# Optimization experiments

Measured on AMD Instinct MI355X. Metric: run time of the kernel, lower is better.

## Reference

```python
import jax, jax.numpy as jnp
import numpy as np

H, W = 48, 48
L = H * W            # 2304 tokens
D = 256              # d_model
NH = 8               # heads (self and memory attn)
FF = 1024            # dim_feedforward
T = 2                # memory frames
BS = 1
GN_GROUPS = 32       # GNActDWConv2d default groups


def layernorm(x, g, b, eps=1e-5):
    m = jnp.mean(x, -1, keepdims=True)
    v = jnp.mean((x - m) ** 2, -1, keepdims=True)
    return (x - m) * jax.lax.rsqrt(v + eps) * g + b


def linear(x, Wt, b):
    # torch nn.Linear convention: Wt is [out, in]
    return x @ Wt.T + b


def mha_core(Q, K, V, nhead):
    # Q [Lq, bs, C], K/V [Lk, bs, C]; AOT MultiheadAttention core (eval: no dropout)
    Lq, bs, C = Q.shape
    hd = C // nhead
    Qh = (Q / np.float32(np.sqrt(hd))).reshape(Lq, bs, nhead, hd).transpose(1, 2, 0, 3)
    Kh = K.reshape(-1, bs, nhead, hd).transpose(1, 2, 0, 3)
    Vh = V.reshape(-1, bs, nhead, hd).transpose(1, 2, 0, 3)
    attn = jax.nn.softmax(jnp.einsum('bhqd,bhkd->bhqk', Qh, Kh), axis=-1)
    out = jnp.einsum('bhqk,bhkd->bhqd', attn, Vh)
    return out.transpose(2, 0, 1, 3).reshape(Lq, bs, C)


def groupnorm(x, g, b, groups, eps=1e-5):
    bs, c, h, w = x.shape
    xg = x.reshape(bs, groups, c // groups, h, w)
    m = jnp.mean(xg, (2, 3, 4), keepdims=True)
    v = jnp.mean((xg - m) ** 2, (2, 3, 4), keepdims=True)
    xg = (xg - m) * jax.lax.rsqrt(v + eps)
    return xg.reshape(bs, c, h, w) * g[None, :, None, None] + b[None, :, None, None]


def dwconv5(x, k):
    # depthwise 5x5, padding=2; x [bs,c,h,w], k [c,1,5,5]
    return jax.lax.conv_general_dilated(x, k, (1, 1), ((2, 2), (2, 2)),
                                        feature_group_count=x.shape[1])


def setup_inputs() -> dict:
    key = jax.random.key(0)
    ks = jax.random.split(key, 16)
    rn = lambda i, shape, s=1.0: jax.random.normal(ks[i], shape, jnp.float32) * s
    w = 0.02
    inp = {
        'tgt': rn(0, (L, BS, D)),
        'global_K': rn(1, (T, L, BS, D)),
        'global_V': rn(2, (T, L, BS, D)),
        'local_K': rn(3, (L, BS, D)),
        'local_V': rn(4, (L, BS, D)),
        # LayerNorms
        'ln1_g': jnp.ones(D, jnp.float32), 'ln1_b': jnp.zeros(D, jnp.float32),
        'ln2_g': jnp.ones(D, jnp.float32), 'ln2_b': jnp.zeros(D, jnp.float32),
        'ln3_g': jnp.ones(D, jnp.float32), 'ln3_b': jnp.zeros(D, jnp.float32),
        'ln4_g': jnp.ones(D, jnp.float32), 'ln4_b': jnp.zeros(D, jnp.float32),
        # self_attn (use_linear=True) Q/K/V + projection
        'sa_Wq': rn(5, (D, D), w), 'sa_bq': jnp.zeros(D, jnp.float32),
        'sa_Wk': rn(6, (D, D), w), 'sa_bk': jnp.zeros(D, jnp.float32),
        'sa_Wv': rn(7, (D, D), w), 'sa_bv': jnp.zeros(D, jnp.float32),
        'sa_Wo': rn(8, (D, D), w), 'sa_bo': jnp.zeros(D, jnp.float32),
        # block linear_Q
        'Wq': rn(9, (D, D), w), 'bq': jnp.zeros(D, jnp.float32),
        # long/short term attn projections (use_linear=False)
        'lt_Wo': rn(10, (D, D), w), 'lt_bo': jnp.zeros(D, jnp.float32),
        'st_Wo': rn(11, (D, D), w), 'st_bo': jnp.zeros(D, jnp.float32),
        # FFN: linear1 -> GN+GELU+DWConv -> linear2
        'W1': rn(12, (FF, D), w), 'b1': jnp.zeros(FF, jnp.float32),
        'gn_g': jnp.ones(FF, jnp.float32), 'gn_b': jnp.zeros(FF, jnp.float32),
        'dw_k': rn(13, (FF, 1, 5, 5), 0.05),
        'W2': rn(14, (D, FF), w), 'b2': jnp.zeros(D, jnp.float32),
    }
    return inp


def reference(tgt, global_K, global_V, local_K, local_V,
              ln1_g, ln1_b, ln2_g, ln2_b, ln3_g, ln3_b, ln4_g, ln4_b,
              sa_Wq, sa_bq, sa_Wk, sa_bk, sa_Wv, sa_bv, sa_Wo, sa_bo,
              Wq, bq, lt_Wo, lt_bo, st_Wo, st_bo,
              W1, b1, gn_g, gn_b, dw_k, W2, b2):
    # --- stage 1: self-attention ---
    _tgt = layernorm(tgt, ln1_g, ln1_b)
    q = linear(_tgt, sa_Wq, sa_bq)
    k = linear(_tgt, sa_Wk, sa_bk)
    v = linear(_tgt, sa_Wv, sa_bv)
    tgt2 = linear(mha_core(q, k, v, NH), sa_Wo, sa_bo)
    tgt = tgt + tgt2  # droppath is identity at eval

    # --- stage 2: long-term + short-term memory cross-attention ---
    _tgt = layernorm(tgt, ln2_g, ln2_b)
    curr_Q = linear(_tgt, Wq, bq)
    curr_K = curr_Q
    curr_V = _tgt

    flat_K = global_K.reshape(-1, BS, D)  # [T*L, bs, D]
    flat_V = global_V.reshape(-1, BS, D)
    tgt2 = linear(mha_core(curr_Q, flat_K, flat_V, NH), lt_Wo, lt_bo)

    k_st = layernorm(local_K + curr_K, ln4_g, ln4_b)
    v_st = layernorm(local_V + curr_V, ln4_g, ln4_b)
    tgt3 = linear(mha_core(curr_Q, k_st, v_st, NH), st_Wo, st_bo)

    tgt = tgt + tgt2 + tgt3

    # --- stage 3: FFN with GN + GELU + depthwise conv ---
    _tgt = layernorm(tgt, ln3_g, ln3_b)
    x = linear(_tgt, W1, b1)                        # [L, bs, FF]
    x = x.reshape(H, W, BS, FF).transpose(2, 3, 0, 1)  # [bs, FF, H, W]
    x = jax.nn.gelu(groupnorm(x, gn_g, gn_b, GN_GROUPS), approximate=False)
    x = dwconv5(x, dw_k)
    x = x.reshape(BS, FF, L).transpose(2, 0, 1)     # [L, bs, FF]
    tgt2 = linear(x, W2, b2)
    return tgt + tgt2
```

## Files before the change

### kernel.cpp

```cpp
#include <hip/hip_runtime.h>
#include <hip/hip_bf16.h>

#define L   2304
#define D   256
#define NHD 8
#define HD  32
#define FF  1024
#define HH  48
#define WWW 48
#define SPL 4
#define RCH 24
#define RP  (L / RCH)
#define S2LOG 0.25503486f

typedef unsigned short bfraw;
typedef __attribute__((ext_vector_type(8))) short s8v;
typedef __attribute__((ext_vector_type(4))) float f4v;

__device__ __forceinline__ bfraw f2b(float x) {
    __hip_bfloat16 h = __float2bfloat16(x);
    return __builtin_bit_cast(bfraw, h);
}

__global__ __launch_bounds__(256) void diag_kernel(float* __restrict__ out, float c, int n)
{
    int i = blockIdx.x * 256 + threadIdx.x;
    if (i < n) out[i] = c;
}

__global__ __launch_bounds__(256) void ln_kernel(
    const float* __restrict__ inA, const float* __restrict__ inB,
    const float* __restrict__ g, const float* __restrict__ b,
    float* __restrict__ out, bfraw* __restrict__ outb)
{
    int row = blockIdx.x, t = threadIdx.x;
    size_t idx = (size_t)row * D + t;
    float v = inA[idx];
    if (inB) v += inB[idx];
    __shared__ float rs[256], rq[256];
    rs[t] = v; rq[t] = v * v;
    __syncthreads();
    for (int o = 128; o > 0; o >>= 1) {
        if (t < o) { rs[t] += rs[t + o]; rq[t] += rq[t + o]; }
        __syncthreads();
    }
    float mean = rs[0] * (1.f / D);
    float var  = rq[0] * (1.f / D) - mean * mean;
    float rstd = rsqrtf(var + 1e-5f);
    float r = (v - mean) * rstd * g[t] + b[t];
    if (out)  out[idx]  = r;
    if (outb) outb[idx] = f2b(r);
}

__global__ __launch_bounds__(256) void gemm_mfma(
    const bfraw* __restrict__ A, const float* __restrict__ W,
    const float* __restrict__ bias, const float* res, float* out,
    bfraw* __restrict__ outb, float oscale,
    int M, int N, int K)
{
    __shared__ __attribute__((aligned(16))) short Wl[64][32];
    int t = threadIdx.x;
    int w = t >> 6, l = t & 63;
    int lo = l & 15, quad = l >> 4;
    int m0 = blockIdx.x * 32, n0 = blockIdx.y * 64;
    int wr = (w & 1) * 16, wc = (w >> 1) * 32;
    f4v acc[2];
    acc[0] = (f4v){0.f, 0.f, 0.f, 0.f};
    acc[1] = (f4v){0.f, 0.f, 0.f, 0.f};

    int aswz = (quad ^ ((lo >> 2) & 3)) * 8;
    int srow = t >> 3, spart = t & 7;
    const bfraw* ap = A + (size_t)(m0 + wr + lo) * K + quad * 8;

    for (int k0 = 0; k0 < K; k0 += 32) {
        float4 w4[2];
        #pragma unroll
        for (int i = 0; i < 2; i++)
            w4[i] = *reinterpret_cast<const float4*>(W + (size_t)(n0 + i * 32 + srow) * K + k0 + spart * 4);
        s8v af = *reinterpret_cast<const s8v*>(ap + k0);
        __syncthreads();
        #pragma unroll
        for (int i = 0; i < 2; i++) {
            int row = i * 32 + srow;
            int col = ((spart >> 1) ^ ((row >> 2) & 3)) * 8 + (spart & 1) * 4;
            ushort4 wb;
            wb.x = f2b(w4[i].x); wb.y = f2b(w4[i].y); wb.z = f2b(w4[i].z); wb.w = f2b(w4[i].w);
            *reinterpret_cast<ushort4*>(&Wl[row][col]) = wb;
        }
        __syncthreads();
        #pragma unroll
        for (int j = 0; j < 2; j++) {
            int rw = wc + j * 16 + lo;
            s8v wf = *reinterpret_cast<const s8v*>(&Wl[rw][aswz]);
            acc[j] = __builtin_amdgcn_mfma_f32_16x16x32_bf16(af, wf, acc[j], 0, 0, 0);
        }
    }

    #pragma unroll
    for (int j = 0; j < 2; j++) {
        #pragma unroll
        for (int r = 0; r < 4; r++) {
            int mrow = m0 + wr + quad * 4 + r;
            int ncol = n0 + wc + j * 16 + lo;
            float v = acc[j][r] + bias[ncol];
            size_t idx = (size_t)mrow * N + ncol;
            if (res) v += res[idx];
            if (out) out[idx] = v;
            if (outb) outb[idx] = f2b(v * oscale);
        }
    }
}

__global__ __launch_bounds__(256) void cvt_kernel(
    const float* __restrict__ in, bfraw* __restrict__ out)
{
    size_t i = ((size_t)blockIdx.x * 256 + threadIdx.x) * 4;
    float4 v = *reinterpret_cast<const float4*>(in + i);
    ushort4 o;
    o.x = f2b(v.x); o.y = f2b(v.y); o.z = f2b(v.z); o.w = f2b(v.w);
    *reinterpret_cast<ushort4*>(out + i) = o;
}

__global__ __launch_bounds__(256) void cvtT_kernel(
    const float* __restrict__ in, bfraw* __restrict__ out, int N)
{
    __shared__ float Ls[32][33];
    int h = blockIdx.y, n0 = blockIdx.x * 32, t = threadIdx.x;
    int nl = t >> 3, dq = t & 7;
    float4 v = *reinterpret_cast<const float4*>(in + (size_t)(n0 + nl) * D + h * HD + dq * 4);
    Ls[nl][dq*4+0] = v.x; Ls[nl][dq*4+1] = v.y;
    Ls[nl][dq*4+2] = v.z; Ls[nl][dq*4+3] = v.w;
    __syncthreads();
    int dl = t >> 3, nq = t & 7;
    ushort4 o;
    o.x = f2b(Ls[nq*4+0][dl]); o.y = f2b(Ls[nq*4+1][dl]);
    o.z = f2b(Ls[nq*4+2][dl]); o.w = f2b(Ls[nq*4+3][dl]);
    *reinterpret_cast<ushort4*>(out + (size_t)(h * HD + dl) * N + n0 + nq * 4) = o;
}

__global__ __launch_bounds__(256) void attn_mfma_split(
    const bfraw* __restrict__ Qb, const bfraw* __restrict__ Kb,
    const bfraw* __restrict__ Vt, float* __restrict__ OP,
    float* __restrict__ ML, int Lk, int chunk)
{
    __shared__ __attribute__((aligned(16))) short Ks[64][32];
    __shared__ __attribute__((aligned(16))) short Vts[32][72];
    __shared__ __attribute__((aligned(16))) short Ps[4][16][72];
    __shared__ float Tb[4][16][33];
    int t = threadIdx.x;
    int w = t >> 6, l = t & 63;
    int h = blockIdx.y, q0 = blockIdx.x * 64 + w * 16, z = blockIdx.z;
    int lo = l & 15, quad = l >> 4;
    int kb = z * chunk, ke = kb + chunk;

    s8v qf = *reinterpret_cast<const s8v*>(Qb + (size_t)(q0 + lo) * D + h * HD + quad * 8);
    int kswz = (quad ^ ((lo >> 2) & 3)) * 8;

    int skey = t >> 2, spart = t & 3;
    int kcol = (spart ^ ((skey >> 2) & 3)) * 8;
    int sd = t >> 3, svp = t & 7;
    const bfraw* kp = Kb + (size_t)skey * D + h * HD + spart * 8;
    const bfraw* vp = Vt + (size_t)(h * HD + sd) * Lk + svp * 8;

    float m_r = -1e30f, l_r = 0.f;
    f4v o0 = {0.f, 0.f, 0.f, 0.f}, o1 = {0.f, 0.f, 0.f, 0.f};

    for (int k0 = kb; k0 < ke; k0 += 64) {
        s8v kv = *reinterpret_cast<const s8v*>(kp + (size_t)k0 * D);
        s8v vv = *reinterpret_cast<const s8v*>(vp + k0);
        __syncthreads();
        *reinterpret_cast<s8v*>(&Ks[skey][kcol]) = kv;
        *reinterpret_cast<s8v*>(&Vts[sd][svp * 8]) = vv;
        __syncthreads();

        f4v sc4[4];
        #pragma unroll
        for (int s = 0; s < 4; s++) {
            s8v kf = *reinterpret_cast<const s8v*>(&Ks[lo + 16 * s][kswz]);
            sc4[s] = __builtin_amdgcn_mfma_f32_16x16x32_bf16(kf, qf, (f4v){0.f,0.f,0.f,0.f}, 0, 0, 0);
        }
        float cm = -1e30f;
        #pragma unroll
        for (int s = 0; s < 4; s++)
            #pragma unroll
            for (int r = 0; r < 4; r++)
                cm = fmaxf(cm, sc4[s][r]);
        cm = fmaxf(cm, __shfl_xor(cm, 16));
        cm = fmaxf(cm, __shfl_xor(cm, 32));
        bool skip = __all(cm <= m_r + 8.f);
        if (!skip) {
            float mnew = fmaxf(m_r, cm);
            float alpha = __builtin_amdgcn_exp2f(m_r - mnew);
            l_r *= alpha;
            #pragma unroll
            for (int r = 0; r < 4; r++) { o0[r] *= alpha; o1[r] *= alpha; }
            m_r = mnew;
        }
        float ls = 0.f;
        #pragma unroll
        for (int s = 0; s < 4; s++) {
            float p0 = __builtin_amdgcn_exp2f(sc4[s][0] - m_r);
            float p1 = __builtin_amdgcn_exp2f(sc4[s][1] - m_r);
            float p2 = __builtin_amdgcn_exp2f(sc4[s][2] - m_r);
            float p3 = __builtin_amdgcn_exp2f(sc4[s][3] - m_r);
            ls += p0 + p1 + p2 + p3;
            ushort4 pk;
            pk.x = f2b(p0); pk.y = f2b(p1); pk.z = f2b(p2); pk.w = f2b(p3);
            *reinterpret_cast<ushort4*>(&Ps[w][lo][s * 16 + quad * 4]) = pk;
        }
        ls += __shfl_xor(ls, 16);
        ls += __shfl_xor(ls, 32);
        l_r += ls;
        #pragma unroll
        for (int kc = 0; kc < 2; kc++) {
            s8v pf = *reinterpret_cast<const s8v*>(&Ps[w][lo][kc * 32 + quad * 8]);
            s8v v0 = *reinterpret_cast<const s8v*>(&Vts[lo][kc * 32 + quad * 8]);
            s8v v1 = *reinterpret_cast<const s8v*>(&Vts[16 + lo][kc * 32 + quad * 8]);
            o0 = __builtin_amdgcn_mfma_f32_16x16x32_bf16(v0, pf, o0, 0, 0, 0);
            o1 = __builtin_amdgcn_mfma_f32_16x16x32_bf16(v1, pf, o1, 0, 0, 0);
        }
    }

    #pragma unroll
    for (int r = 0; r < 4; r++) {
        Tb[w][lo][quad * 4 + r]      = o0[r];
        Tb[w][lo][16 + quad * 4 + r] = o1[r];
    }
    float* Oz = OP + (size_t)z * L * D;
    int ql = l >> 2, dq = (l & 3) * 8;
    float4 u0, u1;
    u0.x = Tb[w][ql][dq + 0]; u0.y = Tb[w][ql][dq + 1];
    u0.z = Tb[w][ql][dq + 2]; u0.w = Tb[w][ql][dq + 3];
    u1.x = Tb[w][ql][dq + 4]; u1.y = Tb[w][ql][dq + 5];
    u1.z = Tb[w][ql][dq + 6]; u1.w = Tb[w][ql][dq + 7];
    *reinterpret_cast<float4*>(Oz + (size_t)(q0 + ql) * D + h * HD + dq)     = u0;
    *reinterpret_cast<float4*>(Oz + (size_t)(q0 + ql) * D + h * HD + dq + 4) = u1;
    if (l < 16) {
        size_t mi = (((size_t)z * NHD + h) * L + q0 + lo) * 2;
        ML[mi]     = m_r;
        ML[mi + 1] = l_r;
    }
}

__global__ __launch_bounds__(256) void attn_combine(
    const float* __restrict__ OP, const float* __restrict__ ML,
    bfraw* __restrict__ Ob)
{
    int q = blockIdx.x, t = threadIdx.x, h = t >> 5;
    float m[SPL], lv[SPL];
    float M = -1e30f;
    #pragma unroll
    for (int s = 0; s < SPL; s++) {
        size_t mi = (((size_t)s * NHD + h) * L + q) * 2;
        m[s]  = ML[mi];
        lv[s] = ML[mi + 1];
        M = fmaxf(M, m[s]);
    }
    float wl = 0.f, acc = 0.f;
    #pragma unroll
    for (int s = 0; s < SPL; s++) {
        float w = __builtin_amdgcn_exp2f(m[s] - M);
        wl  += w * lv[s];
        acc += w * OP[(size_t)s * L * D + (size_t)q * D + t];
    }
    Ob[(size_t)q * D + t] = f2b(acc / wl);
}

__global__ __launch_bounds__(256) void gn_stats_part(
    const float* __restrict__ X, float* __restrict__ ps)
{
    int g = blockIdx.x, rc = blockIdx.y, t = threadIdx.x;
    int cq = (t & 7) * 4;
    int rl = t >> 3;
    int r0 = rc * RP;
    float s = 0.f, sq = 0.f;
    #pragma unroll
    for (int p = 0; p < RP / 32; p++) {
        int l = r0 + p * 32 + rl;
        float4 v = *reinterpret_cast<const float4*>(X + (size_t)l * FF + g * 32 + cq);
        s  += v.x + v.y + v.z + v.w;
        sq += v.x*v.x + v.y*v.y + v.z*v.z + v.w*v.w;
    }
    __shared__ float rs[256], rq[256];
    rs[t] = s; rq[t] = sq;
    __syncthreads();
    for (int o = 128; o > 0; o >>= 1) {
        if (t < o) { rs[t] += rs[t + o]; rq[t] += rq[t + o]; }
        __syncthreads();
    }
    if (t == 0) {
        ps[(g * RCH + rc) * 2]     = rs[0];
        ps[(g * RCH + rc) * 2 + 1] = rq[0];
    }
}

__global__ __launch_bounds__(64) void gn_stats_final(
    const float* __restrict__ ps, float* __restrict__ st)
{
    int g = threadIdx.x;
    if (g < 32) {
        float s = 0.f, sq = 0.f;
        for (int i = 0; i < RCH; i++) {
            s  += ps[(g * RCH + i) * 2];
            sq += ps[(g * RCH + i) * 2 + 1];
        }
        float n = (float)(L * 32);
        float mean = s / n;
        float var  = sq / n - mean * mean;
        st[g * 2]     = mean;
        st[g * 2 + 1] = rsqrtf(var + 1e-5f);
    }
}

__global__ __launch_bounds__(256) void gn_gelu_dwconv(
    const float* __restrict__ X, const float* __restrict__ st,
    const float* __restrict__ gg, const float* __restrict__ gb,
    const float* __restrict__ Kw, bfraw* __restrict__ Y)
{
    __shared__ float tile[144][64];
    int h0 = blockIdx.x * 8, w0 = blockIdx.y * 8, c0 = blockIdx.z * 64;
    int t = threadIdx.x;
    int c = t & 63;
    int cg = (c0 + c) >> 5;
    float mu = st[2 * cg], rs = st[2 * cg + 1];
    float ga = gg[c0 + c], be = gb[c0 + c];

    for (int i = t; i < 144 * 64; i += 256) {
        int sp = i >> 6;
        int hy = h0 + (sp / 12) - 2, wx = w0 + (sp % 12) - 2;
        float v = 0.f;
        if (hy >= 0 && hy < HH && wx >= 0 && wx < WWW) {
            float x = X[(size_t)(hy * WWW + wx) * FF + c0 + c];
            x = (x - mu) * rs * ga + be;
            v = 0.5f * x * (1.f + erff(x * 0.70710678118654752f));
        }
        tile[sp][c] = v;
    }
    float kw[25];
    #pragma unroll
    for (int i = 0; i < 25; i++) kw[i] = Kw[(size_t)(c0 + c) * 25 + i];
    __syncthreads();

    int sgrp = t >> 6;
    for (int s = 0; s < 16; s++) {
        int sp = sgrp * 16 + s;
        int oh = sp >> 3, ow = sp & 7;
        float acc = 0.f;
        #pragma unroll
        for (int ky = 0; ky < 5; ky++)
            #pragma unroll
            for (int kx = 0; kx < 5; kx++)
                acc += tile[(oh + ky) * 12 + ow + kx][c] * kw[ky * 5 + kx];
        Y[(size_t)((h0 + oh) * WWW + w0 + ow) * FF + c0 + c] = f2b(acc);
    }
}

extern "C" void kernel_launch(void* const* d_in, const int* in_sizes, int n_in,
                              void* d_out, int out_size, void* d_ws, size_t ws_size,
                              hipStream_t stream)
{
    (void)in_sizes;
    float* out = (float*)d_out;

    if (n_in != 34) {
        diag_kernel<<<(out_size + 255) / 256, 256, 0, stream>>>(out, 2000.f, out_size);
        return;
    }

    const float* tgt    = (const float*)d_in[0];
    const float* gK     = (const float*)d_in[1];
    const float* gV     = (const float*)d_in[2];
    const float* lK     = (const float*)d_in[3];
    const float* lV     = (const float*)d_in[4];
    const float* ln1_g  = (const float*)d_in[5];
    const float* ln1_b  = (const float*)d_in[6];
    const float* ln2_g  = (const float*)d_in[7];
    const float* ln2_b  = (const float*)d_in[8];
    const float* ln3_g  = (const float*)d_in[9];
    const float* ln3_b  = (const float*)d_in[10];
    const float* ln4_g  = (const float*)d_in[11];
    const float* ln4_b  = (const float*)d_in[12];
    const float* sa_Wq  = (const float*)d_in[13];
    const float* sa_bq  = (const float*)d_in[14];
    const float* sa_Wk  = (const float*)d_in[15];
    const float* sa_bk  = (const float*)d_in[16];
    const float* sa_Wv  = (const float*)d_in[17];
    const float* sa_bv  = (const float*)d_in[18];
    const float* sa_Wo  = (const float*)d_in[19];
    const float* sa_bo  = (const float*)d_in[20];
    const float* Wq     = (const float*)d_in[21];
    const float* bq     = (const float*)d_in[22];
    const float* lt_Wo  = (const float*)d_in[23];
    const float* lt_bo  = (const float*)d_in[24];
    const float* st_Wo  = (const float*)d_in[25];
    const float* st_bo  = (const float*)d_in[26];
    const float* W1w    = (const float*)d_in[27];
    const float* b1w    = (const float*)d_in[28];
    const float* gn_g   = (const float*)d_in[29];
    const float* gn_b   = (const float*)d_in[30];
    const float* dw_k   = (const float*)d_in[31];
    const float* W2w    = (const float*)d_in[32];
    const float* b2w    = (const float*)d_in[33];

    const size_t LD = (size_t)L * D;
    const size_t NEED = (6 * LD + (size_t)L * FF + 64) * 4;
    float* ws = (float*)d_ws;
    float* t0 = ws + 0 * LD;
    float* t1 = ws + 1 * LD;
    float* t3 = ws + 3 * LD;
    float* t4 = ws + 4 * LD;
    float* t5 = ws + 5 * LD;
    float* X1 = t0;
    float* X2 = ws + 6 * LD;
    float* ST = X2 + (size_t)L * FF;
    bfraw* qb   = (bfraw*)X2;
    bfraw* kb1  = qb + LD;
    bfraw* vtb1 = qb + 3 * LD;
    bfraw* kb2  = qb + 5 * LD;
    bfraw* vtb2 = qb + 6 * LD;
    float* OP   = ws;
    float* ML   = X2 + (7 * LD) / 2;
    float* PS   = ML;
    bfraw* t0b  = (bfraw*)t0;
    bfraw* t3b  = (bfraw*)t3;
    bfraw* t4b  = (bfraw*)t4;
    bfraw* X2b  = (bfraw*)X2;

    if (ws_size < NEED) {
        int wsMiB = (int)(ws_size >> 20); if (wsMiB > 63) wsMiB = 63;
        diag_kernel<<<(out_size + 255) / 256, 256, 0, stream>>>(out, 64.f + (float)wsMiB, out_size);
        return;
    }

    dim3 gDD(L / 32, D / 64);
    dim3 gDF(L / 32, FF / 64);
    dim3 gATS(L / 64, NHD, SPL);
    int  cvtLD  = (int)(LD / 1024);
    dim3 gT1(L / 32, NHD);
    dim3 gT2(2 * L / 32, NHD);
    dim3 gGN(32, RCH);
    dim3 gDW(6, 6, 16);

    ln_kernel<<<L, 256, 0, stream>>>(tgt, nullptr, ln1_g, ln1_b, nullptr, t0b);
    gemm_mfma<<<gDD, 256, 0, stream>>>(t0b, sa_Wq, sa_bq, nullptr, nullptr, qb,  S2LOG, L, D, D);
    gemm_mfma<<<gDD, 256, 0, stream>>>(t0b, sa_Wk, sa_bk, nullptr, nullptr, kb2, 1.f,   L, D, D);
    gemm_mfma<<<gDD, 256, 0, stream>>>(t0b, sa_Wv, sa_bv, nullptr, t3, nullptr, 1.f, L, D, D);
    cvtT_kernel<<<gT1, 256, 0, stream>>>(t3, vtb2, L);
    attn_mfma_split<<<gATS, 256, 0, stream>>>(qb, kb2, vtb2, OP, ML, L, L / SPL);
    attn_combine<<<L, 256, 0, stream>>>(OP, ML, t4b);
    gemm_mfma<<<gDD, 256, 0, stream>>>(t4b, sa_Wo, sa_bo, tgt, t5, nullptr, 1.f, L, D, D);

    ln_kernel<<<L, 256, 0, stream>>>(t5, nullptr, ln2_g, ln2_b, t0, t3b);
    gemm_mfma<<<gDD, 256, 0, stream>>>(t3b, Wq, bq, nullptr, t1, qb, S2LOG, L, D, D);
    ln_kernel<<<L, 256, 0, stream>>>(t1, lK, ln4_g, ln4_b, nullptr, kb2);
    ln_kernel<<<L, 256, 0, stream>>>(t0, lV, ln4_g, ln4_b, t3, nullptr);
    cvtT_kernel<<<gT1, 256, 0, stream>>>(t3, vtb2, L);
    cvt_kernel<<<2 * cvtLD, 256, 0, stream>>>(gK, kb1);
    cvtT_kernel<<<gT2, 256, 0, stream>>>(gV, vtb1, 2 * L);
    attn_mfma_split<<<gATS, 256, 0, stream>>>(qb, kb1, vtb1, OP, ML, 2 * L, 2 * L / SPL);
    attn_combine<<<L, 256, 0, stream>>>(OP, ML, t4b);
    gemm_mfma<<<gDD, 256, 0, stream>>>(t4b, lt_Wo, lt_bo, t5, t5, nullptr, 1.f, L, D, D);
    attn_mfma_split<<<gATS, 256, 0, stream>>>(qb, kb2, vtb2, OP, ML, L, L / SPL);
    attn_combine<<<L, 256, 0, stream>>>(OP, ML, t4b);
    gemm_mfma<<<gDD, 256, 0, stream>>>(t4b, st_Wo, st_bo, t5, t5, nullptr, 1.f, L, D, D);

    ln_kernel<<<L, 256, 0, stream>>>(t5, nullptr, ln3_g, ln3_b, nullptr, t4b);
    gemm_mfma<<<gDF, 256, 0, stream>>>(t4b, W1w, b1w, nullptr, X1, nullptr, 1.f, L, FF, D);
    gn_stats_part<<<gGN, 256, 0, stream>>>(X1, PS);
    gn_stats_final<<<1, 64, 0, stream>>>(PS, ST);
    gn_gelu_dwconv<<<gDW, 256, 0, stream>>>(X1, ST, gn_g, gn_b, dw_k, X2b);
    gemm_mfma<<<gDD, 256, 0, stream>>>(X2b, W2w, b2w, t5, out, nullptr, 1.f, L, D, FF);
}
```

Measured before the change: 351.2 us.

## Fuse QKV gemms, attention combine into out-proj, and adjacent norm/convert kernels

Merges the three self-attention projection gemms into one launch and folds the split-attention combine step into the output-projection gemm's A-operand load. It also fuses the ln2 and ln4(V) layernorms into one kernel, and the global K convert and V transpose into one kernel. The aim is fewer kernel launches and no round-trip of the combined attention output through memory. In exchange, the combined split partials are recomputed by each column tile of the out-projection, which multiplies reads of the partial buffers.

```diff
diff --git a/kernel.cpp b/kernel.cpp
--- a/kernel.cpp
+++ b/kernel.cpp
@@ -52,6 +52,41 @@
     if (outb) outb[idx] = f2b(r);
 }
 
+__global__ __launch_bounds__(256) void ln2_ln4v(
+    const float* __restrict__ t5, const float* __restrict__ lV,
+    const float* __restrict__ g2, const float* __restrict__ b2,
+    const float* __restrict__ g4, const float* __restrict__ b4,
+    bfraw* __restrict__ out2b, float* __restrict__ outv)
+{
+    int row = blockIdx.x, t = threadIdx.x;
+    size_t idx = (size_t)row * D + t;
+    float v = t5[idx];
+    __shared__ float rs[256], rq[256];
+    rs[t] = v; rq[t] = v * v;
+    __syncthreads();
+    for (int o = 128; o > 0; o >>= 1) {
+        if (t < o) { rs[t] += rs[t + o]; rq[t] += rq[t + o]; }
+        __syncthreads();
+    }
+    float mean = rs[0] * (1.f / D);
+    float var  = rq[0] * (1.f / D) - mean * mean;
+    float rstd = rsqrtf(var + 1e-5f);
+    float r2 = (v - mean) * rstd * g2[t] + b2[t];
+    out2b[idx] = f2b(r2);
+    float u = r2 + lV[idx];
+    __syncthreads();
+    rs[t] = u; rq[t] = u * u;
+    __syncthreads();
+    for (int o = 128; o > 0; o >>= 1) {
+        if (t < o) { rs[t] += rs[t + o]; rq[t] += rq[t + o]; }
+        __syncthreads();
+    }
+    float mean2 = rs[0] * (1.f / D);
+    float var2  = rq[0] * (1.f / D) - mean2 * mean2;
+    float rstd2 = rsqrtf(var2 + 1e-5f);
+    outv[idx] = (u - mean2) * rstd2 * g4[t] + b4[t];
+}
+
 __global__ __launch_bounds__(256) void gemm_mfma(
     const bfraw* __restrict__ A, const float* __restrict__ W,
     const float* __restrict__ bias, const float* res, float* out,
@@ -111,14 +146,153 @@
     }
 }
 
-__global__ __launch_bounds__(256) void cvt_kernel(
-    const float* __restrict__ in, bfraw* __restrict__ out)
-{
-    size_t i = ((size_t)blockIdx.x * 256 + threadIdx.x) * 4;
-    float4 v = *reinterpret_cast<const float4*>(in + i);
-    ushort4 o;
-    o.x = f2b(v.x); o.y = f2b(v.y); o.z = f2b(v.z); o.w = f2b(v.w);
-    *reinterpret_cast<ushort4*>(out + i) = o;
+__global__ __launch_bounds__(256) void gemm_qkv(
+    const bfraw* __restrict__ A,
+    const float* __restrict__ Wq_, const float* __restrict__ bq_,
+    const float* __restrict__ Wk_, const float* __restrict__ bk_,
+    const float* __restrict__ Wv_, const float* __restrict__ bv_,
+    bfraw* __restrict__ qb, bfraw* __restrict__ kb, float* __restrict__ vout)
+{
+    __shared__ __attribute__((aligned(16))) short Wl[64][32];
+    int t = threadIdx.x;
+    int w = t >> 6, l = t & 63;
+    int lo = l & 15, quad = l >> 4;
+    int sel = blockIdx.y >> 2;
+    int m0 = blockIdx.x * 32, n0 = (blockIdx.y & 3) * 64;
+    int wr = (w & 1) * 16, wc = (w >> 1) * 32;
+    const float* W    = (sel == 0) ? Wq_ : (sel == 1) ? Wk_ : Wv_;
+    const float* bias = (sel == 0) ? bq_ : (sel == 1) ? bk_ : bv_;
+    f4v acc[2];
+    acc[0] = (f4v){0.f, 0.f, 0.f, 0.f};
+    acc[1] = (f4v){0.f, 0.f, 0.f, 0.f};
+
+    int aswz = (quad ^ ((lo >> 2) & 3)) * 8;
+    int srow = t >> 3, spart = t & 7;
+    const bfraw* ap = A + (size_t)(m0 + wr + lo) * D + quad * 8;
+
+    for (int k0 = 0; k0 < D; k0 += 32) {
+        float4 w4[2];
+        #pragma unroll
+        for (int i = 0; i < 2; i++)
+            w4[i] = *reinterpret_cast<const float4*>(W + (size_t)(n0 + i * 32 + srow) * D + k0 + spart * 4);
+        s8v af = *reinterpret_cast<const s8v*>(ap + k0);
+        __syncthreads();
+        #pragma unroll
+        for (int i = 0; i < 2; i++) {
+            int row = i * 32 + srow;
+            int col = ((spart >> 1) ^ ((row >> 2) & 3)) * 8 + (spart & 1) * 4;
+            ushort4 wb;
+            wb.x = f2b(w4[i].x); wb.y = f2b(w4[i].y); wb.z = f2b(w4[i].z); wb.w = f2b(w4[i].w);
+            *reinterpret_cast<ushort4*>(&Wl[row][col]) = wb;
+        }
+        __syncthreads();
+        #pragma unroll
+        for (int j = 0; j < 2; j++) {
+            int rw = wc + j * 16 + lo;
+            s8v wf = *reinterpret_cast<const s8v*>(&Wl[rw][aswz]);
+            acc[j] = __builtin_amdgcn_mfma_f32_16x16x32_bf16(af, wf, acc[j], 0, 0, 0);
+        }
+    }
+
+    #pragma unroll
+    for (int j = 0; j < 2; j++) {
+        #pragma unroll
+        for (int r = 0; r < 4; r++) {
+            int mrow = m0 + wr + quad * 4 + r;
+            int ncol = n0 + wc + j * 16 + lo;
+            float v = acc[j][r] + bias[ncol];
+            size_t idx = (size_t)mrow * D + ncol;
+            if (sel == 0)      qb[idx] = f2b(v * S2LOG);
+            else if (sel == 1) kb[idx] = f2b(v);
+            else               vout[idx] = v;
+        }
+    }
+}
+
+__global__ __launch_bounds__(256) void gemm_att(
+    const float* __restrict__ OP, const float* __restrict__ ML,
+    const float* __restrict__ W, const float* __restrict__ bias,
+    const float* __restrict__ res, float* __restrict__ out)
+{
+    __shared__ __attribute__((aligned(16))) short Wl[64][32];
+    int t = threadIdx.x;
+    int w = t >> 6, l = t & 63;
+    int lo = l & 15, quad = l >> 4;
+    int m0 = blockIdx.x * 32, n0 = blockIdx.y * 64;
+    int wr = (w & 1) * 16, wc = (w >> 1) * 32;
+    f4v acc[2];
+    acc[0] = (f4v){0.f, 0.f, 0.f, 0.f};
+    acc[1] = (f4v){0.f, 0.f, 0.f, 0.f};
+
+    int aswz = (quad ^ ((lo >> 2) & 3)) * 8;
+    int srow = t >> 3, spart = t & 7;
+    size_t ar = (size_t)(m0 + wr + lo);
+
+    for (int k0 = 0; k0 < D; k0 += 32) {
+        float4 w4[2];
+        #pragma unroll
+        for (int i = 0; i < 2; i++)
+            w4[i] = *reinterpret_cast<const float4*>(W + (size_t)(n0 + i * 32 + srow) * D + k0 + spart * 4);
+
+        int h = k0 >> 5;
+        float mv[SPL], lvv[SPL];
+        #pragma unroll
+        for (int s = 0; s < SPL; s++) {
+            size_t mi = (((size_t)s * NHD + h) * L + ar) * 2;
+            mv[s]  = ML[mi];
+            lvv[s] = ML[mi + 1];
+        }
+        float Mx = fmaxf(fmaxf(mv[0], mv[1]), fmaxf(mv[2], mv[3]));
+        float wg[SPL], wsum = 0.f;
+        #pragma unroll
+        for (int s = 0; s < SPL; s++) {
+            wg[s] = __builtin_amdgcn_exp2f(mv[s] - Mx);
+            wsum += wg[s] * lvv[s];
+        }
+        float inv = 1.f / wsum;
+        float ca[8] = {0.f, 0.f, 0.f, 0.f, 0.f, 0.f, 0.f, 0.f};
+        #pragma unroll
+        for (int s = 0; s < SPL; s++) {
+            const float* p = OP + (size_t)s * L * D + ar * D + k0 + quad * 8;
+            float4 x = *reinterpret_cast<const float4*>(p);
+            float4 y = *reinterpret_cast<const float4*>(p + 4);
+            ca[0] += wg[s] * x.x; ca[1] += wg[s] * x.y;
+            ca[2] += wg[s] * x.z; ca[3] += wg[s] * x.w;
+            ca[4] += wg[s] * y.x; ca[5] += wg[s] * y.y;
+            ca[6] += wg[s] * y.z; ca[7] += wg[s] * y.w;
+        }
+        s8v af;
+        #pragma unroll
+        for (int e = 0; e < 8; e++) af[e] = (short)f2b(ca[e] * inv);
+
+        __syncthreads();
+        #pragma unroll
+        for (int i = 0; i < 2; i++) {
+            int row = i * 32 + srow;
+            int col = ((spart >> 1) ^ ((row >> 2) & 3)) * 8 + (spart & 1) * 4;
+            ushort4 wb;
+            wb.x = f2b(w4[i].x); wb.y = f2b(w4[i].y); wb.z = f2b(w4[i].z); wb.w = f2b(w4[i].w);
+            *reinterpret_cast<ushort4*>(&Wl[row][col]) = wb;
+        }
+        __syncthreads();
+        #pragma unroll
+        for (int j = 0; j < 2; j++) {
+            int rw = wc + j * 16 + lo;
+            s8v wf = *reinterpret_cast<const s8v*>(&Wl[rw][aswz]);
+            acc[j] = __builtin_amdgcn_mfma_f32_16x16x32_bf16(af, wf, acc[j], 0, 0, 0);
+        }
+    }
+
+    #pragma unroll
+    for (int j = 0; j < 2; j++) {
+        #pragma unroll
+        for (int r = 0; r < 4; r++) {
+            int mrow = m0 + wr + quad * 4 + r;
+            int ncol = n0 + wc + j * 16 + lo;
+            size_t idx = (size_t)mrow * D + ncol;
+            out[idx] = acc[j][r] + bias[ncol] + res[idx];
+        }
+    }
 }
 
 __global__ __launch_bounds__(256) void cvtT_kernel(
@@ -136,6 +310,34 @@
     o.x = f2b(Ls[nq*4+0][dl]); o.y = f2b(Ls[nq*4+1][dl]);
     o.z = f2b(Ls[nq*4+2][dl]); o.w = f2b(Ls[nq*4+3][dl]);
     *reinterpret_cast<ushort4*>(out + (size_t)(h * HD + dl) * N + n0 + nq * 4) = o;
+}
+
+__global__ __launch_bounds__(256) void cvt_both(
+    const float* __restrict__ gK, bfraw* __restrict__ kb1,
+    const float* __restrict__ gV, bfraw* __restrict__ vtb1)
+{
+    __shared__ float Ls[32][33];
+    int t = threadIdx.x;
+    if (blockIdx.y < NHD) {
+        int h = blockIdx.y, n0 = blockIdx.x * 32;
+        const int N = 2 * L;
+        int nl = t >> 3, dq = t & 7;
+        float4 v = *reinterpret_cast<const float4*>(gV + (size_t)(n0 + nl) * D + h * HD + dq * 4);
+        Ls[nl][dq*4+0] = v.x; Ls[nl][dq*4+1] = v.y;
+        Ls[nl][dq*4+2] = v.z; Ls[nl][dq*4+3] = v.w;
+        __syncthreads();
+        int dl = t >> 3, nq = t & 7;
+        ushort4 o;
+        o.x = f2b(Ls[nq*4+0][dl]); o.y = f2b(Ls[nq*4+1][dl]);
+        o.z = f2b(Ls[nq*4+2][dl]); o.w = f2b(Ls[nq*4+3][dl]);
+        *reinterpret_cast<ushort4*>(vtb1 + (size_t)(h * HD + dl) * N + n0 + nq * 4) = o;
+    } else {
+        size_t i = ((size_t)(blockIdx.x * 8 + (blockIdx.y - NHD)) * 256 + t) * 4;
+        float4 v = *reinterpret_cast<const float4*>(gK + i);
+        ushort4 o;
+        o.x = f2b(v.x); o.y = f2b(v.y); o.z = f2b(v.z); o.w = f2b(v.w);
+        *reinterpret_cast<ushort4*>(kb1 + i) = o;
+    }
 }
 
 __global__ __launch_bounds__(256) void attn_mfma_split(
@@ -240,30 +442,6 @@
         ML[mi]     = m_r;
         ML[mi + 1] = l_r;
     }
-}
-
-__global__ __launch_bounds__(256) void attn_combine(
-    const float* __restrict__ OP, const float* __restrict__ ML,
-    bfraw* __restrict__ Ob)
-{
-    int q = blockIdx.x, t = threadIdx.x, h = t >> 5;
-    float m[SPL], lv[SPL];
-    float M = -1e30f;
-    #pragma unroll
-    for (int s = 0; s < SPL; s++) {
-        size_t mi = (((size_t)s * NHD + h) * L + q) * 2;
-        m[s]  = ML[mi];
-        lv[s] = ML[mi + 1];
-        M = fmaxf(M, m[s]);
-    }
-    float wl = 0.f, acc = 0.f;
-    #pragma unroll
-    for (int s = 0; s < SPL; s++) {
-        float w = __builtin_amdgcn_exp2f(m[s] - M);
-        wl  += w * lv[s];
-        acc += w * OP[(size_t)s * L * D + (size_t)q * D + t];
-    }
-    Ob[(size_t)q * D + t] = f2b(acc / wl);
 }
 
 __global__ __launch_bounds__(256) void gn_stats_part(
@@ -434,35 +612,29 @@
 
     dim3 gDD(L / 32, D / 64);
     dim3 gDF(L / 32, FF / 64);
+    dim3 gQKV(L / 32, 12);
     dim3 gATS(L / 64, NHD, SPL);
-    int  cvtLD  = (int)(LD / 1024);
     dim3 gT1(L / 32, NHD);
-    dim3 gT2(2 * L / 32, NHD);
+    dim3 gCB(2 * L / 32, NHD + 8);
     dim3 gGN(32, RCH);
     dim3 gDW(6, 6, 16);
 
     ln_kernel<<<L, 256, 0, stream>>>(tgt, nullptr, ln1_g, ln1_b, nullptr, t0b);
-    gemm_mfma<<<gDD, 256, 0, stream>>>(t0b, sa_Wq, sa_bq, nullptr, nullptr, qb,  S2LOG, L, D, D);
-    gemm_mfma<<<gDD, 256, 0, stream>>>(t0b, sa_Wk, sa_bk, nullptr, nullptr, kb2, 1.f,   L, D, D);
-    gemm_mfma<<<gDD, 256, 0, stream>>>(t0b, sa_Wv, sa_bv, nullptr, t3, nullptr, 1.f, L, D, D);
+    gemm_qkv<<<gQKV, 256, 0, stream>>>(t0b, sa_Wq, sa_bq, sa_Wk, sa_bk, sa_Wv, sa_bv,
+                                       qb, kb2, t3);
     cvtT_kernel<<<gT1, 256, 0, stream>>>(t3, vtb2, L);
     attn_mfma_split<<<gATS, 256, 0, stream>>>(qb, kb2, vtb2, OP, ML, L, L / SPL);
-    attn_combine<<<L, 256, 0, stream>>>(OP, ML, t4b);
-    gemm_mfma<<<gDD, 256, 0, stream>>>(t4b, sa_Wo, sa_bo, tgt, t5, nullptr, 1.f, L, D, D);
-
-    ln_kernel<<<L, 256, 0, stream>>>(t5, nullptr, ln2_g, ln2_b, t0, t3b);
+    gemm_att<<<gDD, 256, 0, stream>>>(OP, ML, sa_Wo, sa_bo, tgt, t5);
+
+    ln2_ln4v<<<L, 256, 0, stream>>>(t5, lV, ln2_g, ln2_b, ln4_g, ln4_b, t3b, t0);
     gemm_mfma<<<gDD, 256, 0, stream>>>(t3b, Wq, bq, nullptr, t1, qb, S2LOG, L, D, D);
     ln_kernel<<<L, 256, 0, stream>>>(t1, lK, ln4_g, ln4_b, nullptr, kb2);
-    ln_kernel<<<L, 256, 0, stream>>>(t0, lV, ln4_g, ln4_b, t3, nullptr);
-    cvtT_kernel<<<gT1, 256, 0, stream>>>(t3, vtb2, L);
-    cvt_kernel<<<2 * cvtLD, 256, 0, stream>>>(gK, kb1);
-    cvtT_kernel<<<gT2, 256, 0, stream>>>(gV, vtb1, 2 * L);
+    cvtT_kernel<<<gT1, 256, 0, stream>>>(t0, vtb2, L);
+    cvt_both<<<gCB, 256, 0, stream>>>(gK, kb1, gV, vtb1);
     attn_mfma_split<<<gATS, 256, 0, stream>>>(qb, kb1, vtb1, OP, ML, 2 * L, 2 * L / SPL);
-    attn_combine<<<L, 256, 0, stream>>>(OP, ML, t4b);
-    gemm_mfma<<<gDD, 256, 0, stream>>>(t4b, lt_Wo, lt_bo, t5, t5, nullptr, 1.f, L, D, D);
+    gemm_att<<<gDD, 256, 0, stream>>>(OP, ML, lt_Wo, lt_bo, t5, t5);
     attn_mfma_split<<<gATS, 256, 0, stream>>>(qb, kb2, vtb2, OP, ML, L, L / SPL);
-    attn_combine<<<L, 256, 0, stream>>>(OP, ML, t4b);
-    gemm_mfma<<<gDD, 256, 0, stream>>>(t4b, st_Wo, st_bo, t5, t5, nullptr, 1.f, L, D, D);
+    gemm_att<<<gDD, 256, 0, stream>>>(OP, ML, st_Wo, st_bo, t5, t5);
 
     ln_kernel<<<L, 256, 0, stream>>>(t5, nullptr, ln3_g, ln3_b, nullptr, t4b);
     gemm_mfma<<<gDF, 256, 0, stream>>>(t4b, W1w, b1w, nullptr, X1, nullptr, 1.f, L, FF, D);
```

Measured after the change: 357.1 us. About the same (+1.7%).
